# Kernel optimization log

Hardware: AMD Instinct MI355X
Metric: run time of the kernel (lower is better)

## Reference

```python
import jax, jax.numpy as jnp
import numpy as np

PROJ_EPS = 1e-5   # hyperbolic_projection keeps ||x|| <= 1 - PROJ_EPS
MIN_NORM = 1e-15  # numerical floor for norms/denominators
N, D, E, L = 100000, 128, 800000, 2


def _norm(x):
    return jnp.linalg.norm(x, axis=-1, keepdims=True)


def hyperbolic_projection(x):
    n = _norm(x)
    max_n = 1.0 - PROJ_EPS
    scale = jnp.where(n > max_n, max_n / jnp.maximum(n, MIN_NORM), 1.0)
    return x * scale


def exp_map_zero(v):
    n = jnp.maximum(_norm(v), MIN_NORM)
    return jnp.tanh(n) * v / n


def log_map_zero(y):
    n = jnp.maximum(_norm(y), MIN_NORM)
    nc = jnp.clip(n, MIN_NORM, 1.0 - PROJ_EPS)
    return jnp.arctanh(nc) * y / n


def mobius_addition(u, v):
    uu = jnp.sum(u * u, -1, keepdims=True)
    vv = jnp.sum(v * v, -1, keepdims=True)
    uv = jnp.sum(u * v, -1, keepdims=True)
    num = (1.0 + 2.0 * uv + vv) * u + (1.0 - uu) * v
    den = 1.0 + 2.0 * uv + uu * vv
    return num / jnp.maximum(den, MIN_NORM)


def setup_inputs() -> dict:
    key = jax.random.key(0)
    k = jax.random.split(key, 5)
    ent = jax.random.normal(k[0], (N, D), jnp.float32) * 0.1
    W = jax.random.normal(k[1], (L, D, D), jnp.float32) * (1.0 / np.sqrt(D))
    bias = jnp.zeros((L, D), jnp.float32)
    rows = jax.random.randint(k[2], (E,), 0, N)
    cols = jax.random.randint(k[3], (E,), 0, N)
    vals = jax.random.uniform(k[4], (E,), jnp.float32) / 8.0  # ~row-normalized adj values
    return {"ent_embeddings": ent, "W": W, "bias": bias,
            "adj_rows": rows, "adj_cols": cols, "adj_vals": vals}


def _gcn_layer(x, W_l, b_l, rows, cols, vals, use_act):
    # log map to tangent at origin, linear transform
    t = log_map_zero(x)                      # [N, D]
    m = t @ W_l                              # [N, D]
    # sparse adjacency matmul: adj @ m  (COO gather-scale-scatter)
    msg = m[cols] * vals[:, None]            # [E, D]
    agg = jax.ops.segment_sum(msg, rows, num_segments=N)  # [N, D]
    h = hyperbolic_projection(exp_map_zero(agg))
    # hyperbolic bias via mobius addition
    bh = hyperbolic_projection(exp_map_zero(b_l[None, :]))  # [1, D]
    h = hyperbolic_projection(mobius_addition(h, bh))
    if use_act:
        h = hyperbolic_projection(exp_map_zero(jnp.tanh(log_map_zero(h))))
    return h


def reference(ent_embeddings, W, bias, adj_rows, adj_cols, adj_vals):
    x = hyperbolic_projection(ent_embeddings)
    for l in range(L):
        use_act = (l < L - 1)  # tanh on all but last layer
        h = _gcn_layer(x, W[l], bias[l], adj_rows, adj_cols, adj_vals, use_act)
        # mobius residual connection with previous layer output
        x = hyperbolic_projection(mobius_addition(h, x))
    return x
```

## Files before the change

### kernel.cpp

```cpp
#include <hip/hip_runtime.h>
#include <math.h>

#define D 128
#define PROJ_EPS 1e-5f
#define MAX_NN (1.0f - PROJ_EPS)
#define MIN_NORM 1e-15f
#define ROWS_PER_BLOCK 2048

struct __align__(8) Edge { int c; float v; };

typedef __attribute__((ext_vector_type(8))) short bf16x8;
typedef __attribute__((ext_vector_type(4))) float f32x4;

__device__ inline unsigned short f2bf(float f) {
    unsigned u = __float_as_uint(f);
    unsigned r = (u + 0x7FFFu + ((u >> 16) & 1u)) >> 16;
    return (unsigned short)r;
}
__device__ inline float bf2f(unsigned short h) {
    return __uint_as_float(((unsigned)h) << 16);
}

__device__ inline float wave_sum(float v) {
#pragma unroll
    for (int off = 32; off; off >>= 1) v += __shfl_xor(v, off, 64);
    return v;
}
__device__ inline float gsum(float v) {
#pragma unroll
    for (int off = 16; off; off >>= 1) v += __shfl_xor(v, off, 64);
    return v;
}
__device__ inline void gsum2(float& a, float& b) {
#pragma unroll
    for (int off = 16; off; off >>= 1) {
        a += __shfl_xor(a, off, 64);
        b += __shfl_xor(b, off, 64);
    }
}
__device__ inline float frcp(float x) { return __builtin_amdgcn_rcpf(x); }
__device__ inline float fsqrt_(float x) { return __builtin_amdgcn_sqrtf(x); }
__device__ inline float tanh_pos(float x) {
    float e = __expf(-2.f * x);
    return (1.f - e) * frcp(1.f + e);
}
__device__ inline float tanh_sgn(float x) {
    float ax = fabsf(x);
    float e = __expf(-2.f * ax);
    float r = (1.f - e) * frcp(1.f + e);
    return copysignf(r, x);
}
__device__ inline float atanh_clip(float x) {
    return 0.5f * __logf((1.f + x) * frcp(1.f - x));
}
__device__ inline void bf4_fma(uint2 g, float v, float& a0, float& a1, float& a2, float& a3) {
    float f0 = __uint_as_float(g.x << 16);
    float f1 = __uint_as_float(g.x & 0xffff0000u);
    float f2 = __uint_as_float(g.y << 16);
    float f3 = __uint_as_float(g.y & 0xffff0000u);
    a0 = fmaf(v, f0, a0); a1 = fmaf(v, f1, a1);
    a2 = fmaf(v, f2, a2); a3 = fmaf(v, f3, a3);
}

__global__ void hist_kernel(const int* __restrict__ rows, int* __restrict__ counts, int e) {
    int i = blockIdx.x * blockDim.x + threadIdx.x;
    if (i < e) atomicAdd(&counts[rows[i]], 1);
}

__global__ __launch_bounds__(256) void partial_kernel(const int* __restrict__ counts,
                                                      int* __restrict__ partials, int n) {
    int t = threadIdx.x;
    int start = blockIdx.x * ROWS_PER_BLOCK + t * 8;
    int s = 0;
#pragma unroll
    for (int j = 0; j < 8; ++j) {
        int i = start + j;
        if (i < n) s += counts[i];
    }
    int lane = t & 63, wv = t >> 6;
#pragma unroll
    for (int o = 32; o; o >>= 1) s += __shfl_xor(s, o, 64);
    __shared__ int wsum[4];
    if (lane == 0) wsum[wv] = s;
    __syncthreads();
    if (t == 0) partials[blockIdx.x] = wsum[0] + wsum[1] + wsum[2] + wsum[3];
}

__global__ void scan_partials(int* __restrict__ partials, int npart) {
    __shared__ int buf[1024];
    int t = threadIdx.x;
    int v = (t < npart) ? partials[t] : 0;
    buf[t] = v;
    __syncthreads();
    for (int o = 1; o < 1024; o <<= 1) {
        int x = (t >= o) ? buf[t - o] : 0;
        __syncthreads();
        buf[t] += x;
        __syncthreads();
    }
    if (t < npart) partials[t] = buf[t] - v;
}

__global__ __launch_bounds__(256) void rowptr_kernel(const int* __restrict__ counts,
                                                     const int* __restrict__ partials,
                                                     int* __restrict__ row_ptr,
                                                     int* __restrict__ cursor, int n, int e) {
    int t = threadIdx.x;
    int start = blockIdx.x * ROWS_PER_BLOCK + t * 8;
    int c[8];
    int s = 0;
#pragma unroll
    for (int j = 0; j < 8; ++j) {
        int i = start + j;
        c[j] = (i < n) ? counts[i] : 0;
        s += c[j];
    }
    int lane = t & 63, wv = t >> 6;
    int inc = s;
#pragma unroll
    for (int o = 1; o < 64; o <<= 1) {
        int tt = __shfl_up(inc, o, 64);
        if (lane >= o) inc += tt;
    }
    __shared__ int wsum[4];
    if (lane == 63) wsum[wv] = inc;
    __syncthreads();
    if (t == 0) {
        int acc = 0;
        for (int w = 0; w < 4; ++w) { int tmp = wsum[w]; wsum[w] = acc; acc += tmp; }
    }
    __syncthreads();
    int run = partials[blockIdx.x] + wsum[wv] + (inc - s);
#pragma unroll
    for (int j = 0; j < 8; ++j) {
        int i = start + j;
        if (i < n) {
            row_ptr[i] = run;
            cursor[i] = run;
            run += c[j];
        }
    }
    if (blockIdx.x == 0 && t == 0) row_ptr[n] = e;
}

__global__ void scatter_kernel(const int* __restrict__ rows, const int* __restrict__ cols,
                               const float* __restrict__ vals, int* __restrict__ cursor,
                               Edge* __restrict__ eds, int e) {
    int i = blockIdx.x * blockDim.x + threadIdx.x;
    if (i < e) {
        int r = rows[i];
        int pos = atomicAdd(&cursor[r], 1);
        Edge ed; ed.c = cols[i]; ed.v = vals[i];
        eds[pos] = ed;
    }
}

__global__ __launch_bounds__(256) void proj_init(const float* __restrict__ ent,
                                                 float* __restrict__ x,
                                                 float* __restrict__ logscale,
                                                 float* __restrict__ xnorm2, int n) {
    int wid = (int)((blockIdx.x * (size_t)blockDim.x + threadIdx.x) >> 6);
    int lane = threadIdx.x & 63;
    if (wid >= n) return;
    float2 v = *(const float2*)(ent + (size_t)wid * D + 2 * lane);
    float nrm = sqrtf(wave_sum(v.x * v.x + v.y * v.y));
    float scale = (nrm > MAX_NN) ? MAX_NN / fmaxf(nrm, MIN_NORM) : 1.0f;
    float px = v.x * scale, py = v.y * scale;
    float n2 = fmaxf(sqrtf(wave_sum(px * px + py * py)), MIN_NORM);
    float nc = fminf(fmaxf(n2, MIN_NORM), MAX_NN);
    float ls = atanhf(nc) / n2;
    *(float2*)(x + (size_t)wid * D + 2 * lane) = make_float2(px, py);
    if (lane == 0) { logscale[wid] = ls; xnorm2[wid] = n2 * n2; }
}

__global__ void bias_prep(const float* __restrict__ bias, float* __restrict__ bh,
                          float* __restrict__ vvb) {
    int l = blockIdx.x;
    int lane = threadIdx.x;
    float2 b2 = *(const float2*)(bias + (size_t)l * D + 2 * lane);
    float nn = fmaxf(sqrtf(wave_sum(b2.x * b2.x + b2.y * b2.y)), MIN_NORM);
    float s = tanhf(nn) / nn;
    float bx = b2.x * s, by = b2.y * s;
    float pn = sqrtf(wave_sum(bx * bx + by * by));
    float sc = (pn > MAX_NN) ? MAX_NN / fmaxf(pn, MIN_NORM) : 1.0f;
    bx *= sc; by *= sc;
    float vv = wave_sum(bx * bx + by * by);
    *(float2*)(bh + (size_t)l * D + 2 * lane) = make_float2(bx, by);
    if (lane == 0) vvb[l] = vv;
}

__global__ __launch_bounds__(256, 3) void logmap_gemm(const float* __restrict__ x,
                                                      const float* __restrict__ logscale,
                                                      const float* __restrict__ W,
                                                      unsigned short* __restrict__ m, int n,
                                                      int ntiles) {
    __shared__ char lds[16384];
    const int t = threadIdx.x;
    const int wid = t >> 6, lane = t & 63;
    const int lcol = lane & 15, lkg = lane >> 4;
    const int colbase = wid * 32;

    bf16x8 Bh[4][2], Bl[4][2];
#pragma unroll
    for (int ki = 0; ki < 4; ++ki) {
#pragma unroll
        for (int cf = 0; cf < 2; ++cf) {
            const float* wp = W + (size_t)(ki * 32 + lkg * 8) * D + colbase + cf * 16 + lcol;
#pragma unroll
            for (int e = 0; e < 8; ++e) {
                float f = wp[(size_t)e * D];
                unsigned short h = f2bf(f);
                Bh[ki][cf][e] = (short)h;
                Bl[ki][cf][e] = (short)f2bf(f - bf2f(h));
            }
        }
    }

    for (int tile = blockIdx.x; tile < ntiles; tile += gridDim.x) {
        const int row0 = tile * 32;
        __syncthreads();
#pragma unroll
        for (int p = t; p < 512; p += 256) {
            int fi = p >> 6, ln = p & 63;
            int rf = fi >> 2, ki = fi & 3;
            int row = row0 + rf * 16 + (ln & 15);
            int k0 = ki * 32 + (ln >> 4) * 8;
            float v[8];
            if (row < n) {
                float ls = logscale[row];
                const float* xp = x + (size_t)row * D + k0;
                *(float4*)&v[0] = *(const float4*)xp;
                *(float4*)&v[4] = *(const float4*)(xp + 4);
#pragma unroll
                for (int e = 0; e < 8; ++e) v[e] *= ls;
            } else {
#pragma unroll
                for (int e = 0; e < 8; ++e) v[e] = 0.f;
            }
            bf16x8 hi, lo;
#pragma unroll
            for (int e = 0; e < 8; ++e) {
                unsigned short h = f2bf(v[e]);
                hi[e] = (short)h;
                lo[e] = (short)f2bf(v[e] - bf2f(h));
            }
            *(bf16x8*)(lds + fi * 1024 + ln * 16) = hi;
            *(bf16x8*)(lds + 8192 + fi * 1024 + ln * 16) = lo;
        }
        __syncthreads();

        f32x4 acc[2][2];
#pragma unroll
        for (int rf = 0; rf < 2; ++rf)
#pragma unroll
            for (int cf = 0; cf < 2; ++cf) acc[rf][cf] = (f32x4){0.f, 0.f, 0.f, 0.f};

#pragma unroll
        for (int ki = 0; ki < 4; ++ki) {
            bf16x8 Ah[2], Al[2];
#pragma unroll
            for (int rf = 0; rf < 2; ++rf) {
                Ah[rf] = *(const bf16x8*)(lds + (rf * 4 + ki) * 1024 + lane * 16);
                Al[rf] = *(const bf16x8*)(lds + 8192 + (rf * 4 + ki) * 1024 + lane * 16);
            }
#pragma unroll
            for (int rf = 0; rf < 2; ++rf)
#pragma unroll
                for (int cf = 0; cf < 2; ++cf) {
                    acc[rf][cf] = __builtin_amdgcn_mfma_f32_16x16x32_bf16(Ah[rf], Bh[ki][cf], acc[rf][cf], 0, 0, 0);
                    acc[rf][cf] = __builtin_amdgcn_mfma_f32_16x16x32_bf16(Ah[rf], Bl[ki][cf], acc[rf][cf], 0, 0, 0);
                    acc[rf][cf] = __builtin_amdgcn_mfma_f32_16x16x32_bf16(Al[rf], Bh[ki][cf], acc[rf][cf], 0, 0, 0);
                }
        }

#pragma unroll
        for (int rf = 0; rf < 2; ++rf)
#pragma unroll
            for (int cf = 0; cf < 2; ++cf)
#pragma unroll
                for (int r = 0; r < 4; ++r) {
                    int row = row0 + rf * 16 + lkg * 4 + r;
                    if (row < n)
                        m[(size_t)row * D + colbase + cf * 16 + lcol] = f2bf(acc[rf][cf][r]);
                }
    }
}

__global__ __launch_bounds__(256) void aggregate(const unsigned short* __restrict__ m,
                                                 const int* __restrict__ row_ptr,
                                                 const Edge* __restrict__ eds,
                                                 const float* __restrict__ bh,
                                                 const float* __restrict__ vvb_p,
                                                 float* __restrict__ x,
                                                 float* __restrict__ logscale,
                                                 float* __restrict__ xnorm2,
                                                 int n, int use_act, int last) {
    int wv = (int)((blockIdx.x * (size_t)blockDim.x + threadIdx.x) >> 6);
    int lane = threadIdx.x & 63;
    int half = lane >> 5, li = lane & 31;
    int r = wv * 2 + half;
    if (wv * 2 >= n) return;
    bool active = (r < n);

    int beg = 0, end = 0;
    if (active) { beg = row_ptr[r]; end = row_ptr[r + 1]; }

    const char* mB = (const char*)m + ((size_t)li << 3);
    float a0 = 0.f, a1 = 0.f, a2 = 0.f, a3 = 0.f;
    int e = beg;
    for (; e + 4 <= end; e += 4) {
        Edge e0 = eds[e], e1 = eds[e + 1], e2 = eds[e + 2], e3 = eds[e + 3];
        uint2 g0 = *(const uint2*)(mB + ((size_t)e0.c << 8));
        uint2 g1 = *(const uint2*)(mB + ((size_t)e1.c << 8));
        uint2 g2 = *(const uint2*)(mB + ((size_t)e2.c << 8));
        uint2 g3 = *(const uint2*)(mB + ((size_t)e3.c << 8));
        bf4_fma(g0, e0.v, a0, a1, a2, a3);
        bf4_fma(g1, e1.v, a0, a1, a2, a3);
        bf4_fma(g2, e2.v, a0, a1, a2, a3);
        bf4_fma(g3, e3.v, a0, a1, a2, a3);
    }
    for (; e < end; ++e) {
        Edge ee = eds[e];
        uint2 g = *(const uint2*)(mB + ((size_t)ee.c << 8));
        bf4_fma(g, ee.v, a0, a1, a2, a3);
    }

    float4 bhv = *(const float4*)(bh + 4 * li);
    float vvb = *vvb_p;

    float saa = a0 * a0 + a1 * a1 + a2 * a2 + a3 * a3;
    float sab = a0 * bhv.x + a1 * bhv.y + a2 * bhv.z + a3 * bhv.w;
    gsum2(saa, sab);

    float na = fmaxf(fsqrt_(saa), MIN_NORM);
    float th = tanh_pos(na);
    float s1 = th * frcp(na);
    float nh = th;
    if (th > MAX_NN) { s1 *= MAX_NN * frcp(th); nh = MAX_NN; }
    float h0 = a0 * s1, h1 = a1 * s1, h2_ = a2 * s1, h3_ = a3 * s1;
    float uu = nh * nh;
    float uv = s1 * sab;

    float ca = 1.f + 2.f * uv + vvb;
    float cb = 1.f - uu;
    float den = fmaxf(1.f + 2.f * uv + uu * vvb, MIN_NORM);
    float nsq = fmaxf(ca * ca * uu + 2.f * ca * cb * uv + cb * cb * vvb, 0.f);
    float rden = frcp(den);
    float n2 = fsqrt_(nsq) * rden;
    float s2 = rden;
    if (n2 > MAX_NN) { s2 *= MAX_NN * frcp(n2); n2 = MAX_NN; }
    float p0 = (ca * h0 + cb * bhv.x) * s2;
    float p1 = (ca * h1 + cb * bhv.y) * s2;
    float p2 = (ca * h2_ + cb * bhv.z) * s2;
    float p3 = (ca * h3_ + cb * bhv.w) * s2;

    float4 xo = active ? *(const float4*)(x + (size_t)r * D + 4 * li)
                       : make_float4(0.f, 0.f, 0.f, 0.f);

    float q0, q1, q2, q3, uu3, uv3;
    if (use_act) {
        float nnv = fmaxf(n2, MIN_NORM);
        float nc = fminf(fmaxf(n2, MIN_NORM), MAX_NN);
        float ls2 = atanh_clip(nc) * frcp(nnv);
        float t0 = tanh_sgn(p0 * ls2);
        float t1 = tanh_sgn(p1 * ls2);
        float t2 = tanh_sgn(p2 * ls2);
        float t3 = tanh_sgn(p3 * ls2);
        float stt = t0 * t0 + t1 * t1 + t2 * t2 + t3 * t3;
        float stx = t0 * xo.x + t1 * xo.y + t2 * xo.z + t3 * xo.w;
        gsum2(stt, stx);
        float n3 = fmaxf(fsqrt_(stt), MIN_NORM);
        float th3 = tanh_pos(n3);
        float s3 = th3 * frcp(n3);
        float nh3 = th3;
        if (th3 > MAX_NN) { s3 *= MAX_NN * frcp(th3); nh3 = MAX_NN; }
        q0 = t0 * s3; q1 = t1 * s3; q2 = t2 * s3; q3 = t3 * s3;
        uu3 = nh3 * nh3;
        uv3 = s3 * stx;
    } else {
        float suv = gsum(p0 * xo.x + p1 * xo.y + p2 * xo.z + p3 * xo.w);
        q0 = p0; q1 = p1; q2 = p2; q3 = p3;
        uu3 = n2 * n2;
        uv3 = suv;
    }

    float vv = active ? xnorm2[r] : 0.f;
    ca = 1.f + 2.f * uv3 + vv;
    cb = 1.f - uu3;
    den = fmaxf(1.f + 2.f * uv3 + uu3 * vv, MIN_NORM);
    nsq = fmaxf(ca * ca * uu3 + 2.f * ca * cb * uv3 + cb * cb * vv, 0.f);
    rden = frcp(den);
    float n4 = fsqrt_(nsq) * rden;
    float s4 = rden;
    if (n4 > MAX_NN) { s4 *= MAX_NN * frcp(n4); n4 = MAX_NN; }
    float o0 = (ca * q0 + cb * xo.x) * s4;
    float o1 = (ca * q1 + cb * xo.y) * s4;
    float o2 = (ca * q2 + cb * xo.z) * s4;
    float o3 = (ca * q3 + cb * xo.w) * s4;

    if (active) {
        *(float4*)(x + (size_t)r * D + 4 * li) = make_float4(o0, o1, o2, o3);
        if (li == 0) {
            xnorm2[r] = n4 * n4;
            if (!last) {
                float nnv = fmaxf(n4, MIN_NORM);
                float nc = fminf(fmaxf(n4, MIN_NORM), MAX_NN);
                logscale[r] = atanh_clip(nc) * frcp(nnv);
            }
        }
    }
}

extern "C" void kernel_launch(void* const* d_in, const int* in_sizes, int n_in,
                              void* d_out, int out_size, void* d_ws, size_t ws_size,
                              hipStream_t stream) {
    const float* ent  = (const float*)d_in[0];
    const float* W    = (const float*)d_in[1];
    const float* bias = (const float*)d_in[2];
    const int* rows   = (const int*)d_in[3];
    const int* cols   = (const int*)d_in[4];
    const float* vals = (const float*)d_in[5];
    float* x = (float*)d_out;

    const int n = in_sizes[0] / D;
    const int e = in_sizes[3];
    const int nlayers = in_sizes[1] / (D * D);
    const int npart = (n + ROWS_PER_BLOCK - 1) / ROWS_PER_BLOCK;
    const int ntiles = (n + 31) / 32;

    char* ws = (char*)d_ws;
    size_t off = 0;
    auto alloc = [&](size_t bytes) {
        void* p = ws + off;
        off += (bytes + 255) & ~(size_t)255;
        return p;
    };
    unsigned short* m = (unsigned short*)alloc((size_t)n * D * sizeof(unsigned short));
    float* logscale = (float*)alloc((size_t)n * sizeof(float));
    float* xnorm2   = (float*)alloc((size_t)n * sizeof(float));
    int*   counts   = (int*)alloc((size_t)n * sizeof(int));
    int*   row_ptr  = (int*)alloc((size_t)(n + 1) * sizeof(int));
    int*   cursor   = (int*)alloc((size_t)n * sizeof(int));
    int*   partials = (int*)alloc((size_t)(npart > 1024 ? npart : 1024) * sizeof(int));
    float* bhb      = (float*)alloc((size_t)nlayers * D * sizeof(float));
    float* vvb      = (float*)alloc((size_t)nlayers * sizeof(float));
    Edge*  eds      = (Edge*)alloc((size_t)e * sizeof(Edge));

    hipMemsetAsync(counts, 0, (size_t)n * sizeof(int), stream);
    hist_kernel<<<(e + 255) / 256, 256, 0, stream>>>(rows, counts, e);
    partial_kernel<<<npart, 256, 0, stream>>>(counts, partials, n);
    scan_partials<<<1, 1024, 0, stream>>>(partials, npart);
    rowptr_kernel<<<npart, 256, 0, stream>>>(counts, partials, row_ptr, cursor, n, e);
    scatter_kernel<<<(e + 255) / 256, 256, 0, stream>>>(rows, cols, vals, cursor, eds, e);

    bias_prep<<<nlayers, 64, 0, stream>>>(bias, bhb, vvb);
    proj_init<<<(n + 3) / 4, 256, 0, stream>>>(ent, x, logscale, xnorm2, n);

    for (int l = 0; l < nlayers; ++l) {
        logmap_gemm<<<782, 256, 0, stream>>>(x, logscale, W + (size_t)l * D * D, m, n, ntiles);
        int use_act = (l < nlayers - 1) ? 1 : 0;
        aggregate<<<(n + 7) / 8, 256, 0, stream>>>(m, row_ptr, eds, bhb + (size_t)l * D,
                                                   vvb + l, x, logscale, xnorm2, n,
                                                   use_act, (l == nlayers - 1) ? 1 : 0);
    }
}
```

Baseline: 288.1 us.

## Sort rows by degree for balanced aggregation and use packed FP32 math

Adds a degree histogram, scan and scatter that build a permutation grouping rows of equal degree, so the two half-waves in each wave walk edge lists of similar length. The aggregation loop is unrolled to 8 edges and the per-lane arithmetic is rewritten with inline v_pk_fma_f32/v_pk_mul_f32 packed instructions. The aim is less divergence and tail idling from uneven row degrees, plus fewer VALU instructions. The cost is three extra preprocessing launches and an extra permutation indirection, which also scatters the x/row_ptr accesses.

```diff
diff --git a/kernel.cpp b/kernel.cpp
--- a/kernel.cpp
+++ b/kernel.cpp
@@ -6,6 +6,7 @@
 #define MAX_NN (1.0f - PROJ_EPS)
 #define MIN_NORM 1e-15f
 #define ROWS_PER_BLOCK 2048
+#define NDEG 64
 
 struct __align__(8) Edge { int c; float v; };
 
@@ -53,13 +54,23 @@
 __device__ inline float atanh_clip(float x) {
     return 0.5f * __logf((1.f + x) * frcp(1.f - x));
 }
-__device__ inline void bf4_fma(uint2 g, float v, float& a0, float& a1, float& a2, float& a3) {
-    float f0 = __uint_as_float(g.x << 16);
-    float f1 = __uint_as_float(g.x & 0xffff0000u);
-    float f2 = __uint_as_float(g.y << 16);
-    float f3 = __uint_as_float(g.y & 0xffff0000u);
-    a0 = fmaf(v, f0, a0); a1 = fmaf(v, f1, a1);
-    a2 = fmaf(v, f2, a2); a3 = fmaf(v, f3, a3);
+
+__device__ inline float2 mk2(float a, float b) { float2 r; r.x = a; r.y = b; return r; }
+__device__ inline float2 bc2(float a) { return mk2(a, a); }
+__device__ inline float2 pk_fma2(float2 a, float2 b, float2 c) {
+    float2 d;
+    asm("v_pk_fma_f32 %0, %1, %2, %3" : "=v"(d) : "v"(a), "v"(b), "v"(c));
+    return d;
+}
+__device__ inline float2 pk_mul2(float2 a, float2 b) {
+    float2 d;
+    asm("v_pk_mul_f32 %0, %1, %2" : "=v"(d) : "v"(a), "v"(b));
+    return d;
+}
+__device__ inline float2 up2(unsigned u) {
+    uint2 t; t.x = u << 16; t.y = u & 0xffff0000u;
+    float2 r; r.x = __uint_as_float(t.x); r.y = __uint_as_float(t.y);
+    return r;
 }
 
 __global__ void hist_kernel(const int* __restrict__ rows, int* __restrict__ counts, int e) {
@@ -152,6 +163,26 @@
         int pos = atomicAdd(&cursor[r], 1);
         Edge ed; ed.c = cols[i]; ed.v = vals[i];
         eds[pos] = ed;
+    }
+}
+
+__global__ void deg_hist(const int* __restrict__ counts, int* __restrict__ dh, int n) {
+    int i = blockIdx.x * blockDim.x + threadIdx.x;
+    if (i < n) atomicAdd(&dh[min(counts[i], NDEG - 1)], 1);
+}
+__global__ void deg_scan(const int* __restrict__ dh, int* __restrict__ dcur) {
+    if (threadIdx.x == 0) {
+        int s = 0;
+        for (int j = 0; j < NDEG; ++j) { int v = dh[j]; dcur[j] = s; s += v; }
+    }
+}
+__global__ void deg_scatter(const int* __restrict__ counts, int* __restrict__ dcur,
+                            int* __restrict__ perm, int n) {
+    int i = blockIdx.x * blockDim.x + threadIdx.x;
+    if (i < n) {
+        int d = min(counts[i], NDEG - 1);
+        int p = atomicAdd(&dcur[d], 1);
+        perm[p] = i;
     }
 }
 
@@ -289,6 +320,7 @@
 __global__ __launch_bounds__(256) void aggregate(const unsigned short* __restrict__ m,
                                                  const int* __restrict__ row_ptr,
                                                  const Edge* __restrict__ eds,
+                                                 const int* __restrict__ perm,
                                                  const float* __restrict__ bh,
                                                  const float* __restrict__ vvb_p,
                                                  float* __restrict__ x,
@@ -298,38 +330,44 @@
     int wv = (int)((blockIdx.x * (size_t)blockDim.x + threadIdx.x) >> 6);
     int lane = threadIdx.x & 63;
     int half = lane >> 5, li = lane & 31;
-    int r = wv * 2 + half;
     if (wv * 2 >= n) return;
-    bool active = (r < n);
+    int idx = wv * 2 + half;
+    bool active = (idx < n);
+    int r = active ? perm[idx] : 0;
 
     int beg = 0, end = 0;
     if (active) { beg = row_ptr[r]; end = row_ptr[r + 1]; }
 
     const char* mB = (const char*)m + ((size_t)li << 3);
-    float a0 = 0.f, a1 = 0.f, a2 = 0.f, a3 = 0.f;
+    float2 A01 = bc2(0.f), A23 = bc2(0.f);
     int e = beg;
-    for (; e + 4 <= end; e += 4) {
-        Edge e0 = eds[e], e1 = eds[e + 1], e2 = eds[e + 2], e3 = eds[e + 3];
-        uint2 g0 = *(const uint2*)(mB + ((size_t)e0.c << 8));
-        uint2 g1 = *(const uint2*)(mB + ((size_t)e1.c << 8));
-        uint2 g2 = *(const uint2*)(mB + ((size_t)e2.c << 8));
-        uint2 g3 = *(const uint2*)(mB + ((size_t)e3.c << 8));
-        bf4_fma(g0, e0.v, a0, a1, a2, a3);
-        bf4_fma(g1, e1.v, a0, a1, a2, a3);
-        bf4_fma(g2, e2.v, a0, a1, a2, a3);
-        bf4_fma(g3, e3.v, a0, a1, a2, a3);
+    for (; e + 8 <= end; e += 8) {
+#pragma unroll
+        for (int j = 0; j < 8; j += 4) {
+            Edge e0 = eds[e + j], e1 = eds[e + j + 1], e2 = eds[e + j + 2], e3 = eds[e + j + 3];
+            uint2 g0 = *(const uint2*)(mB + ((size_t)(unsigned)e0.c << 8));
+            uint2 g1 = *(const uint2*)(mB + ((size_t)(unsigned)e1.c << 8));
+            uint2 g2 = *(const uint2*)(mB + ((size_t)(unsigned)e2.c << 8));
+            uint2 g3 = *(const uint2*)(mB + ((size_t)(unsigned)e3.c << 8));
+            A01 = pk_fma2(up2(g0.x), bc2(e0.v), A01); A23 = pk_fma2(up2(g0.y), bc2(e0.v), A23);
+            A01 = pk_fma2(up2(g1.x), bc2(e1.v), A01); A23 = pk_fma2(up2(g1.y), bc2(e1.v), A23);
+            A01 = pk_fma2(up2(g2.x), bc2(e2.v), A01); A23 = pk_fma2(up2(g2.y), bc2(e2.v), A23);
+            A01 = pk_fma2(up2(g3.x), bc2(e3.v), A01); A23 = pk_fma2(up2(g3.y), bc2(e3.v), A23);
+        }
     }
     for (; e < end; ++e) {
         Edge ee = eds[e];
-        uint2 g = *(const uint2*)(mB + ((size_t)ee.c << 8));
-        bf4_fma(g, ee.v, a0, a1, a2, a3);
-    }
-
-    float4 bhv = *(const float4*)(bh + 4 * li);
+        uint2 g = *(const uint2*)(mB + ((size_t)(unsigned)ee.c << 8));
+        A01 = pk_fma2(up2(g.x), bc2(ee.v), A01); A23 = pk_fma2(up2(g.y), bc2(ee.v), A23);
+    }
+
+    float4 bhv4 = *(const float4*)(bh + 4 * li);
+    float2 b01 = mk2(bhv4.x, bhv4.y), b23 = mk2(bhv4.z, bhv4.w);
     float vvb = *vvb_p;
 
-    float saa = a0 * a0 + a1 * a1 + a2 * a2 + a3 * a3;
-    float sab = a0 * bhv.x + a1 * bhv.y + a2 * bhv.z + a3 * bhv.w;
+    float2 daa = pk_fma2(A23, A23, pk_mul2(A01, A01));
+    float2 dab = pk_fma2(A23, b23, pk_mul2(A01, b01));
+    float saa = daa.x + daa.y, sab = dab.x + dab.y;
     gsum2(saa, sab);
 
     float na = fmaxf(fsqrt_(saa), MIN_NORM);
@@ -337,7 +375,7 @@
     float s1 = th * frcp(na);
     float nh = th;
     if (th > MAX_NN) { s1 *= MAX_NN * frcp(th); nh = MAX_NN; }
-    float h0 = a0 * s1, h1 = a1 * s1, h2_ = a2 * s1, h3_ = a3 * s1;
+    float2 H01 = pk_mul2(A01, bc2(s1)), H23 = pk_mul2(A23, bc2(s1));
     float uu = nh * nh;
     float uv = s1 * sab;
 
@@ -349,37 +387,38 @@
     float n2 = fsqrt_(nsq) * rden;
     float s2 = rden;
     if (n2 > MAX_NN) { s2 *= MAX_NN * frcp(n2); n2 = MAX_NN; }
-    float p0 = (ca * h0 + cb * bhv.x) * s2;
-    float p1 = (ca * h1 + cb * bhv.y) * s2;
-    float p2 = (ca * h2_ + cb * bhv.z) * s2;
-    float p3 = (ca * h3_ + cb * bhv.w) * s2;
-
-    float4 xo = active ? *(const float4*)(x + (size_t)r * D + 4 * li)
-                       : make_float4(0.f, 0.f, 0.f, 0.f);
-
-    float q0, q1, q2, q3, uu3, uv3;
+    float2 P01 = pk_mul2(pk_fma2(H01, bc2(ca), pk_mul2(b01, bc2(cb))), bc2(s2));
+    float2 P23 = pk_mul2(pk_fma2(H23, bc2(ca), pk_mul2(b23, bc2(cb))), bc2(s2));
+
+    float4 xo4 = active ? *(const float4*)(x + (size_t)r * D + 4 * li)
+                        : make_float4(0.f, 0.f, 0.f, 0.f);
+    float2 xo01 = mk2(xo4.x, xo4.y), xo23 = mk2(xo4.z, xo4.w);
+
+    float2 Q01, Q23;
+    float uu3, uv3;
     if (use_act) {
         float nnv = fmaxf(n2, MIN_NORM);
         float nc = fminf(fmaxf(n2, MIN_NORM), MAX_NN);
         float ls2 = atanh_clip(nc) * frcp(nnv);
-        float t0 = tanh_sgn(p0 * ls2);
-        float t1 = tanh_sgn(p1 * ls2);
-        float t2 = tanh_sgn(p2 * ls2);
-        float t3 = tanh_sgn(p3 * ls2);
-        float stt = t0 * t0 + t1 * t1 + t2 * t2 + t3 * t3;
-        float stx = t0 * xo.x + t1 * xo.y + t2 * xo.z + t3 * xo.w;
+        float2 Z01 = pk_mul2(P01, bc2(ls2)), Z23 = pk_mul2(P23, bc2(ls2));
+        float2 T01 = mk2(tanh_sgn(Z01.x), tanh_sgn(Z01.y));
+        float2 T23 = mk2(tanh_sgn(Z23.x), tanh_sgn(Z23.y));
+        float2 dtt = pk_fma2(T23, T23, pk_mul2(T01, T01));
+        float2 dtx = pk_fma2(T23, xo23, pk_mul2(T01, xo01));
+        float stt = dtt.x + dtt.y, stx = dtx.x + dtx.y;
         gsum2(stt, stx);
         float n3 = fmaxf(fsqrt_(stt), MIN_NORM);
         float th3 = tanh_pos(n3);
         float s3 = th3 * frcp(n3);
         float nh3 = th3;
         if (th3 > MAX_NN) { s3 *= MAX_NN * frcp(th3); nh3 = MAX_NN; }
-        q0 = t0 * s3; q1 = t1 * s3; q2 = t2 * s3; q3 = t3 * s3;
+        Q01 = pk_mul2(T01, bc2(s3)); Q23 = pk_mul2(T23, bc2(s3));
         uu3 = nh3 * nh3;
         uv3 = s3 * stx;
     } else {
-        float suv = gsum(p0 * xo.x + p1 * xo.y + p2 * xo.z + p3 * xo.w);
-        q0 = p0; q1 = p1; q2 = p2; q3 = p3;
+        float2 dpx = pk_fma2(P23, xo23, pk_mul2(P01, xo01));
+        float suv = gsum(dpx.x + dpx.y);
+        Q01 = P01; Q23 = P23;
         uu3 = n2 * n2;
         uv3 = suv;
     }
@@ -393,13 +432,11 @@
     float n4 = fsqrt_(nsq) * rden;
     float s4 = rden;
     if (n4 > MAX_NN) { s4 *= MAX_NN * frcp(n4); n4 = MAX_NN; }
-    float o0 = (ca * q0 + cb * xo.x) * s4;
-    float o1 = (ca * q1 + cb * xo.y) * s4;
-    float o2 = (ca * q2 + cb * xo.z) * s4;
-    float o3 = (ca * q3 + cb * xo.w) * s4;
+    float2 O01 = pk_mul2(pk_fma2(Q01, bc2(ca), pk_mul2(xo01, bc2(cb))), bc2(s4));
+    float2 O23 = pk_mul2(pk_fma2(Q23, bc2(ca), pk_mul2(xo23, bc2(cb))), bc2(s4));
 
     if (active) {
-        *(float4*)(x + (size_t)r * D + 4 * li) = make_float4(o0, o1, o2, o3);
+        *(float4*)(x + (size_t)r * D + 4 * li) = make_float4(O01.x, O01.y, O23.x, O23.y);
         if (li == 0) {
             xnorm2[r] = n4 * n4;
             if (!last) {
@@ -442,16 +479,23 @@
     int*   row_ptr  = (int*)alloc((size_t)(n + 1) * sizeof(int));
     int*   cursor   = (int*)alloc((size_t)n * sizeof(int));
     int*   partials = (int*)alloc((size_t)(npart > 1024 ? npart : 1024) * sizeof(int));
+    int*   dh       = (int*)alloc((size_t)NDEG * sizeof(int));
+    int*   dcur     = (int*)alloc((size_t)NDEG * sizeof(int));
+    int*   perm     = (int*)alloc((size_t)n * sizeof(int));
     float* bhb      = (float*)alloc((size_t)nlayers * D * sizeof(float));
     float* vvb      = (float*)alloc((size_t)nlayers * sizeof(float));
     Edge*  eds      = (Edge*)alloc((size_t)e * sizeof(Edge));
 
     hipMemsetAsync(counts, 0, (size_t)n * sizeof(int), stream);
+    hipMemsetAsync(dh, 0, (size_t)NDEG * sizeof(int), stream);
     hist_kernel<<<(e + 255) / 256, 256, 0, stream>>>(rows, counts, e);
     partial_kernel<<<npart, 256, 0, stream>>>(counts, partials, n);
     scan_partials<<<1, 1024, 0, stream>>>(partials, npart);
     rowptr_kernel<<<npart, 256, 0, stream>>>(counts, partials, row_ptr, cursor, n, e);
     scatter_kernel<<<(e + 255) / 256, 256, 0, stream>>>(rows, cols, vals, cursor, eds, e);
+    deg_hist<<<(n + 255) / 256, 256, 0, stream>>>(counts, dh, n);
+    deg_scan<<<1, 64, 0, stream>>>(dh, dcur);
+    deg_scatter<<<(n + 255) / 256, 256, 0, stream>>>(counts, dcur, perm, n);
 
     bias_prep<<<nlayers, 64, 0, stream>>>(bias, bhb, vvb);
     proj_init<<<(n + 3) / 4, 256, 0, stream>>>(ent, x, logscale, xnorm2, n);
@@ -459,7 +503,7 @@
     for (int l = 0; l < nlayers; ++l) {
         logmap_gemm<<<782, 256, 0, stream>>>(x, logscale, W + (size_t)l * D * D, m, n, ntiles);
         int use_act = (l < nlayers - 1) ? 1 : 0;
-        aggregate<<<(n + 7) / 8, 256, 0, stream>>>(m, row_ptr, eds, bhb + (size_t)l * D,
+        aggregate<<<(n + 7) / 8, 256, 0, stream>>>(m, row_ptr, eds, perm, bhb + (size_t)l * D,
                                                    vvb + l, x, logscale, xnorm2, n,
                                                    use_act, (l == nlayers - 1) ? 1 : 0);
     }
```

Measured after the change: 992.0 us. +244.4%, slower.
